# Kernel optimization log

Hardware: AMD Instinct MI355X
Metric: run time of the kernel (lower is better)

Reference implementation:

```python
import jax, jax.numpy as jnp
import numpy as np

NUM_WIRES = 20
DEPTH = 4


def setup_inputs() -> dict:
    key = jax.random.key(0)
    x = jax.random.normal(key, (NUM_WIRES,), dtype=jnp.float32)
    return {"x": x}


def _apply_1q(state, gate, wire):
    # state: flat [2^n] complex; apply 2x2 gate on `wire`
    s = state.reshape(2 ** wire, 2, -1)
    return jnp.einsum('ab,ibj->iaj', gate, s).reshape(-1)


def _apply_cnot(state, control):
    # CNOT on adjacent wires (control, control+1): flip target where control==1
    s = state.reshape(2 ** control, 2, 2, -1)
    s = jnp.concatenate([s[:, :1], s[:, 1:, ::-1]], axis=1)
    return s.reshape(-1)


def _simulate(x):
    n = NUM_WIRES
    state = jnp.zeros(2 ** n, dtype=jnp.complex64).at[0].set(1.0)
    half = (x.astype(jnp.float32) * 0.5)
    c = jnp.cos(half).astype(jnp.complex64)  # [n]
    s = jnp.sin(half).astype(jnp.complex64)  # [n]
    for _ in range(DEPTH):
        for w in range(n):
            cw, sw = c[w], s[w]
            rx = jnp.stack([jnp.stack([cw, -1j * sw]), jnp.stack([-1j * sw, cw])])
            ry = jnp.stack([jnp.stack([cw, -sw]), jnp.stack([sw, cw])])
            state = _apply_1q(state, rx, w)
            state = _apply_1q(state, ry, w)
        for w in range(n - 1):
            state = _apply_cnot(state, w)
    probs = jnp.abs(state) ** 2  # real float32 [2^n]
    expz = []
    for i in range(n):
        p = probs.reshape(2 ** i, 2, -1).sum(axis=(0, 2))
        expz.append(p[0] - p[1])
    return jnp.stack(expz).astype(jnp.float32)  # [n] <Z_i>


def reference(x):
    return _simulate(x)
```

## Files before the change

### kernel.cpp

```cpp
#include <hip/hip_runtime.h>


#define NW 20

__device__ __forceinline__ float2 cmul(float2 a, float2 b) {
    return make_float2(a.x*b.x - a.y*b.y, a.x*b.y + a.y*b.x);
}

__device__ __forceinline__ void apply_gate(float2& a0, float2& a1,
                                           float2 u00, float2 u01,
                                           float2 u10, float2 u11) {
    float2 b0, b1;
    b0.x = u00.x*a0.x - u00.y*a0.y + u01.x*a1.x - u01.y*a1.y;
    b0.y = u00.x*a0.y + u00.y*a0.x + u01.x*a1.y + u01.y*a1.x;
    b1.x = u10.x*a0.x - u10.y*a0.y + u11.x*a1.x - u11.y*a1.y;
    b1.y = u10.x*a0.y + u10.y*a0.x + u11.x*a1.y + u11.y*a1.x;
    a0 = b0; a1 = b1;
}

__device__ __forceinline__ float2 shflx(float2 v, int m) {
    float2 r;
    r.x = __shfl_xor(v.x, m, 64);
    r.y = __shfl_xor(v.y, m, 64);
    return r;
}

__device__ __forceinline__ unsigned sfx(unsigned x) {
    x ^= x >> 1; x ^= x >> 2; x ^= x >> 4; x ^= x >> 8; x ^= x >> 16; return x;
}

template<int A>
__device__ __forceinline__ void gate_regbit(float2 (&amp)[4], const float2* Gw) {
    float2 u00 = Gw[0], u01 = Gw[1], u10 = Gw[2], u11 = Gw[3];
    #pragma unroll
    for (int r = 0; r < 4; r++)
        if (!(r & (1 << A)))
            apply_gate(amp[r], amp[r | (1 << A)], u00, u01, u10, u11);
}

template<int A, int LM>
__device__ __forceinline__ void swap_reg_lane4(float2 (&amp)[4], unsigned lane) {
    bool hb = (lane & (unsigned)LM) != 0u;
    #pragma unroll
    for (int r = 0; r < 4; r++) {
        if (!(r & (1 << A))) {
            float2 lo = amp[r], hi = amp[r | (1 << A)];
            float2 xs = hb ? lo : hi;
            float2 ys = shflx(xs, LM);
            amp[r]            = hb ? ys : lo;
            amp[r | (1 << A)] = hb ? hi : ys;
        }
    }
}

__device__ __forceinline__ void prep_Gs(const float* __restrict__ x, float2* Gs,
                                        unsigned t) {
    if (t < NW) {
        float h = 0.5f * x[t];
        float c = cosf(h), s = sinf(h);
        float cc = c*c, ss = s*s, cs = c*s;
        Gs[t*4+0] = make_float2(cc,  ss);
        Gs[t*4+1] = make_float2(-cs, -cs);
        Gs[t*4+2] = make_float2(cs,  -cs);
        Gs[t*4+3] = make_float2(cc,  -ss);
    }
}

template<int MODE>
__global__ __launch_bounds__(1024) void stageA(const float* __restrict__ x,
                                               const float2* __restrict__ src,
                                               float2* __restrict__ dst) {
    __shared__ float2 lds[4096];
    __shared__ float2 Gs[4*NW];
    const unsigned t = threadIdx.x;
    const unsigned lane = t & 63u, wv = t >> 6;
    const unsigned w0 = wv & 1u, w1 = (wv >> 1) & 1u, w2 = (wv >> 2) & 1u, w3 = wv >> 3;
    const unsigned l4v = (lane >> 4) & 1u, l5v = lane >> 5;
    const unsigned H   = blockIdx.x;
    const unsigned Hp  = H ^ (H >> 1);
    const unsigned inj = (H & 1u) << 11;
    const unsigned lb  = (wv << 8) | (lane << 2);
    const unsigned gb  = (lb ^ (lb >> 1)) ^ inj;

    float4 q0, q1;
    if (MODE == 1) {
        const float4* q = (const float4*)(src + ((size_t)Hp << 12) + (gb & ~3u));
        q0 = q[0]; q1 = q[1];
    }
    prep_Gs(x, Gs, t);
    __syncthreads();

    float2 amp[4];
    if (MODE == 1) {
        float2 e0 = make_float2(q0.x,q0.y), e1 = make_float2(q0.z,q0.w);
        float2 e2 = make_float2(q1.x,q1.y), e3 = make_float2(q1.z,q1.w);
        bool s2 = (gb & 2u) != 0u;
        amp[0] = s2 ? e2 : e0;
        amp[1] = s2 ? e3 : e1;
        amp[2] = s2 ? e1 : e3;
        amp[3] = s2 ? e0 : e2;
    } else {
        float2 P = make_float2(1.0f, 0.0f);
        #pragma unroll
        for (int b = 12; b <= 19; b++)
            P = cmul(P, Gs[(19-b)*4 + (int)((Hp >> (b-12)) & 1u)*2]);
        #pragma unroll
        for (int b = 2; b <= 11; b++)
            P = cmul(P, Gs[(19-b)*4 + (int)((gb >> b) & 1u)*2]);
        float2 T[4];
        #pragma unroll
        for (int j = 0; j < 4; j++)
            T[j] = cmul(P, cmul(Gs[19*4 + (j&1)*2], Gs[18*4 + ((j>>1)&1)*2]));
        bool s2 = (gb & 2u) != 0u;
        amp[0] = s2 ? T[2] : T[0];
        amp[1] = s2 ? T[3] : T[1];
        amp[2] = s2 ? T[1] : T[3];
        amp[3] = s2 ? T[0] : T[2];
    }

    gate_regbit<0>(amp, Gs + 19*4);
    gate_regbit<1>(amp, Gs + 18*4);
    swap_reg_lane4<0,1>(amp, lane);
    swap_reg_lane4<1,2>(amp, lane);
    gate_regbit<0>(amp, Gs + 17*4);
    gate_regbit<1>(amp, Gs + 16*4);
    swap_reg_lane4<0,4>(amp, lane);
    swap_reg_lane4<1,8>(amp, lane);
    gate_regbit<0>(amp, Gs + 15*4);
    gate_regbit<1>(amp, Gs + 14*4);
    swap_reg_lane4<0,16>(amp, lane);
    swap_reg_lane4<1,32>(amp, lane);
    gate_regbit<0>(amp, Gs + 13*4);
    gate_regbit<1>(amp, Gs + 12*4);
    #pragma unroll
    for (int k = 0; k < 4; k++) lds[lane | ((unsigned)k << 6) | (wv << 8)] = amp[k];
    __syncthreads();
    #pragma unroll
    for (int k = 0; k < 4; k++)
        amp[k] = lds[(lane & 15u) | (w0 << 4) | (w1 << 5) | (w2 << 6) | (w3 << 7)
                     | ((unsigned)(k & 1) << 8) | ((unsigned)(k >> 1) << 9)
                     | (l4v << 10) | (l5v << 11)];
    gate_regbit<0>(amp, Gs + 11*4);
    gate_regbit<1>(amp, Gs + 10*4);
    swap_reg_lane4<0,16>(amp, lane);
    gate_regbit<0>(amp, Gs + 9*4);
    swap_reg_lane4<1,32>(amp, lane);
    gate_regbit<1>(amp, Gs + 8*4);
    float2* d = dst + ((size_t)H << 12);
    #pragma unroll
    for (int k = 0; k < 4; k++)
        d[(lane & 15u) | (w0 << 4) | (w1 << 5) | (w2 << 6) | (w3 << 7)
          | (l4v << 8) | (l5v << 9)
          | ((unsigned)(k & 1) << 10) | ((unsigned)(k >> 1) << 11)] = amp[k];
}

template<int FUSE>
__global__ __launch_bounds__(1024) void stageB(const float* __restrict__ x,
                                               float2* __restrict__ st,
                                               float* __restrict__ partial) {
    __shared__ float2 lds[4096];
    __shared__ float2 Gs[4*NW];
    const unsigned t = threadIdx.x;
    const unsigned lane = t & 63u, wv = t >> 6;
    const unsigned w0 = wv & 1u, w1 = (wv >> 1) & 1u, w2 = (wv >> 2) & 1u, w3 = wv >> 3;
    const unsigned m = lane & 15u, l4v = (lane >> 4) & 1u, l5v = lane >> 5;
    const unsigned bb = blockIdx.x;

    float2 amp[4];
    const unsigned lbase = m | (bb << 4) | (l4v << 14) | (l5v << 15)
                         | (w0 << 16) | (w1 << 17) | (w2 << 18) | (w3 << 19);
    #pragma unroll
    for (int k = 0; k < 4; k++)
        amp[k] = st[lbase | ((unsigned)(k & 1) << 12) | ((unsigned)(k >> 1) << 13)];
    prep_Gs(x, Gs, t);
    __syncthreads();

    gate_regbit<0>(amp, Gs + 7*4);
    gate_regbit<1>(amp, Gs + 6*4);
    swap_reg_lane4<0,16>(amp, lane);
    swap_reg_lane4<1,32>(amp, lane);
    gate_regbit<0>(amp, Gs + 5*4);
    gate_regbit<1>(amp, Gs + 4*4);
    #pragma unroll
    for (int k = 0; k < 4; k++) lds[lane | ((unsigned)k << 6) | (wv << 8)] = amp[k];
    __syncthreads();
    #pragma unroll
    for (int k = 0; k < 4; k++)
        amp[k] = lds[(lane & 15u) | (w0 << 4) | (w1 << 5) | (w2 << 6) | (w3 << 7)
                     | ((unsigned)(k & 1) << 8) | ((unsigned)(k >> 1) << 9)
                     | (l4v << 10) | (l5v << 11)];
    gate_regbit<0>(amp, Gs + 3*4);
    gate_regbit<1>(amp, Gs + 2*4);
    swap_reg_lane4<0,16>(amp, lane);
    gate_regbit<0>(amp, Gs + 1*4);
    swap_reg_lane4<1,32>(amp, lane);
    gate_regbit<1>(amp, Gs + 0*4);

    if (!FUSE) {
        #pragma unroll
        for (int k = 0; k < 4; k++)
            st[m | (bb << 4) | (w0 << 12) | (w1 << 13) | (w2 << 14) | (w3 << 15)
               | (l4v << 16) | (l5v << 17)
               | ((unsigned)(k & 1) << 18) | ((unsigned)(k >> 1) << 19)] = amp[k];
    } else {
        float p[4];
        #pragma unroll
        for (int k = 0; k < 4; k++) p[k] = amp[k].x*amp[k].x + amp[k].y*amp[k].y;
        float S19 = (p[0] + p[1]) - (p[2] + p[3]);
        float D   = p[0] - p[1] - p[2] + p[3];
        unsigned v = m | (bb << 4) | (w0 << 12) | (w1 << 13) | (w2 << 14)
                   | (w3 << 15) | (l4v << 16) | (l5v << 17);
        unsigned cm = sfx(v);
        float acc[NW];
        acc[0] = S19; acc[1] = D;
        #pragma unroll
        for (int w = 2; w < NW; w++)
            acc[w] = ((cm >> (19 - w)) & 1u) ? -D : D;

        __syncthreads();
        float* red = (float*)lds;
        #pragma unroll
        for (int w = 0; w < NW; w++) {
            float s = acc[w];
            #pragma unroll
            for (int off = 32; off; off >>= 1) s += __shfl_down(s, off, 64);
            if (lane == 0) red[wv*NW + w] = s;
        }
        __syncthreads();
        if (t < NW) {
            float s = 0.0f;
            #pragma unroll
            for (int v16 = 0; v16 < 16; v16++) s += red[v16*NW + (int)t];
            partial[bb*NW + t] = s;
        }
    }
}

__global__ __launch_bounds__(256) void reduce_out(const float* __restrict__ partial,
                                                  float* __restrict__ out) {
    __shared__ float red[4*NW];
    unsigned t = threadIdx.x;
    float vals[NW];
    #pragma unroll
    for (int w = 0; w < NW; w++) vals[w] = partial[t*NW + w];
    #pragma unroll
    for (int w = 0; w < NW; w++) {
        float v = vals[w];
        #pragma unroll
        for (int off = 32; off; off >>= 1) v += __shfl_down(v, off, 64);
        if ((t & 63u) == 0u) red[(t >> 6)*NW + w] = v;
    }
    __syncthreads();
    if (t < NW) out[t] = red[t] + red[NW+t] + red[2*NW+t] + red[3*NW+t];
}

extern "C" void kernel_launch(void* const* d_in, const int* in_sizes, int n_in,
                              void* d_out, int out_size, void* d_ws, size_t ws_size,
                              hipStream_t stream) {
    (void)in_sizes; (void)n_in; (void)out_size; (void)ws_size;
    const float* x = (const float*)d_in[0];
    float* out = (float*)d_out;

    char* ws = (char*)d_ws;
    float*  partial = (float*)(ws + 1024);
    float2* buf0    = (float2*)(ws + 65536);
    float2* buf1    = (float2*)(ws + 65536 + (size_t)(8u << 20));

    stageA<0><<<256, 1024, 0, stream>>>(x, buf1 , buf0);
    stageB<0><<<256, 1024, 0, stream>>>(x, buf0, nullptr);
    stageA<1><<<256, 1024, 0, stream>>>(x, buf0, buf1);
    stageB<0><<<256, 1024, 0, stream>>>(x, buf1, nullptr);
    stageA<1><<<256, 1024, 0, stream>>>(x, buf1, buf0);
    stageB<1><<<256, 1024, 0, stream>>>(x, buf0, partial);
    reduce_out<<<1, 256, 0, stream>>>(partial, out);
}
```

Baseline: 73.37 us.

## Remap qubit-to-lane layout for vectorized global access and swizzled LDS transposes

Reworks the bit-to-thread mapping in both stages. Stage B now loads and stores state with float4 accesses on paired amplitudes and applies gates only on register bit 1, with more lane swaps. Its LDS transpose gets an XOR swizzle to avoid bank conflicts. Stage A replaces lane shuffles with a second LDS transpose so its global writes are contiguous per lane. The aim is to cut global memory transactions and LDS bank conflicts, at the cost of an extra barrier and LDS round trip in stage A and changed reduction bookkeeping in the fused path.

```diff
diff --git a/kernel.cpp b/kernel.cpp
--- a/kernel.cpp
+++ b/kernel.cpp
@@ -66,6 +66,10 @@
     }
 }
 
+__device__ __forceinline__ unsigned swz(unsigned a) {
+    return a ^ (((a >> 9) & 7u) << 3);
+}
+
 template<int MODE>
 __global__ __launch_bounds__(1024) void stageA(const float* __restrict__ x,
                                                const float2* __restrict__ src,
@@ -75,7 +79,6 @@
     const unsigned t = threadIdx.x;
     const unsigned lane = t & 63u, wv = t >> 6;
     const unsigned w0 = wv & 1u, w1 = (wv >> 1) & 1u, w2 = (wv >> 2) & 1u, w3 = wv >> 3;
-    const unsigned l4v = (lane >> 4) & 1u, l5v = lane >> 5;
     const unsigned H   = blockIdx.x;
     const unsigned Hp  = H ^ (H >> 1);
     const unsigned inj = (H & 1u) << 11;
@@ -137,21 +140,22 @@
     __syncthreads();
     #pragma unroll
     for (int k = 0; k < 4; k++)
-        amp[k] = lds[(lane & 15u) | (w0 << 4) | (w1 << 5) | (w2 << 6) | (w3 << 7)
-                     | ((unsigned)(k & 1) << 8) | ((unsigned)(k >> 1) << 9)
-                     | (l4v << 10) | (l5v << 11)];
+        amp[k] = lds[lane | (w0 << 6) | (w1 << 7) | ((unsigned)k << 8) | (w2 << 10) | (w3 << 11)];
     gate_regbit<0>(amp, Gs + 11*4);
     gate_regbit<1>(amp, Gs + 10*4);
-    swap_reg_lane4<0,16>(amp, lane);
+    __syncthreads();
+    #pragma unroll
+    for (int k = 0; k < 4; k++) lds[lane | ((unsigned)k << 6) | (wv << 8)] = amp[k];
+    __syncthreads();
+    #pragma unroll
+    for (int k = 0; k < 4; k++)
+        amp[k] = lds[lane | (w2 << 6) | (w3 << 7) | (w0 << 8) | (w1 << 9) | ((unsigned)k << 10)];
     gate_regbit<0>(amp, Gs + 9*4);
-    swap_reg_lane4<1,32>(amp, lane);
     gate_regbit<1>(amp, Gs + 8*4);
     float2* d = dst + ((size_t)H << 12);
     #pragma unroll
     for (int k = 0; k < 4; k++)
-        d[(lane & 15u) | (w0 << 4) | (w1 << 5) | (w2 << 6) | (w3 << 7)
-          | (l4v << 8) | (l5v << 9)
-          | ((unsigned)(k & 1) << 10) | ((unsigned)(k >> 1) << 11)] = amp[k];
+        d[lane | (w0 << 6) | (w1 << 7) | (w2 << 8) | (w3 << 9) | ((unsigned)k << 10)] = amp[k];
 }
 
 template<int FUSE>
@@ -163,59 +167,68 @@
     const unsigned t = threadIdx.x;
     const unsigned lane = t & 63u, wv = t >> 6;
     const unsigned w0 = wv & 1u, w1 = (wv >> 1) & 1u, w2 = (wv >> 2) & 1u, w3 = wv >> 3;
-    const unsigned m = lane & 15u, l4v = (lane >> 4) & 1u, l5v = lane >> 5;
+    const unsigned l012 = lane & 7u;
+    const unsigned l3 = (lane >> 3) & 1u, l4 = (lane >> 4) & 1u, l5 = lane >> 5;
     const unsigned bb = blockIdx.x;
 
+    float4 qa, qb;
+    {
+        const unsigned ba = (l012 << 1) | (bb << 4) | (l3 << 13) | (l4 << 14)
+                          | (l5 << 15) | (w0 << 16) | (w1 << 17) | (w2 << 18) | (w3 << 19);
+        qa = *(const float4*)(st + ba);
+        qb = *(const float4*)(st + (ba | (1u << 12)));
+    }
+    prep_Gs(x, Gs, t);
+    __syncthreads();
+
     float2 amp[4];
-    const unsigned lbase = m | (bb << 4) | (l4v << 14) | (l5v << 15)
-                         | (w0 << 16) | (w1 << 17) | (w2 << 18) | (w3 << 19);
-    #pragma unroll
-    for (int k = 0; k < 4; k++)
-        amp[k] = st[lbase | ((unsigned)(k & 1) << 12) | ((unsigned)(k >> 1) << 13)];
-    prep_Gs(x, Gs, t);
-    __syncthreads();
-
-    gate_regbit<0>(amp, Gs + 7*4);
+    amp[0] = make_float2(qa.x, qa.y); amp[1] = make_float2(qa.z, qa.w);
+    amp[2] = make_float2(qb.x, qb.y); amp[3] = make_float2(qb.z, qb.w);
+
+    gate_regbit<1>(amp, Gs + 7*4);
+    swap_reg_lane4<1,8>(amp, lane);
     gate_regbit<1>(amp, Gs + 6*4);
-    swap_reg_lane4<0,16>(amp, lane);
+    swap_reg_lane4<1,16>(amp, lane);
+    gate_regbit<1>(amp, Gs + 5*4);
     swap_reg_lane4<1,32>(amp, lane);
-    gate_regbit<0>(amp, Gs + 5*4);
     gate_regbit<1>(amp, Gs + 4*4);
     #pragma unroll
-    for (int k = 0; k < 4; k++) lds[lane | ((unsigned)k << 6) | (wv << 8)] = amp[k];
-    __syncthreads();
-    #pragma unroll
-    for (int k = 0; k < 4; k++)
-        amp[k] = lds[(lane & 15u) | (w0 << 4) | (w1 << 5) | (w2 << 6) | (w3 << 7)
-                     | ((unsigned)(k & 1) << 8) | ((unsigned)(k >> 1) << 9)
-                     | (l4v << 10) | (l5v << 11)];
-    gate_regbit<0>(amp, Gs + 3*4);
+    for (int k = 0; k < 4; k++)
+        lds[swz(lane | ((unsigned)k << 6) | (wv << 8))] = amp[k];
+    __syncthreads();
+    #pragma unroll
+    for (int k = 0; k < 4; k++)
+        amp[k] = lds[swz(l012 | (w0 << 3) | (w1 << 4) | (w2 << 5)
+                         | ((unsigned)(k & 1) << 6) | (w3 << 7)
+                         | ((unsigned)(k >> 1) << 8)
+                         | (l3 << 9) | (l4 << 10) | (l5 << 11))];
+    gate_regbit<1>(amp, Gs + 3*4);
+    swap_reg_lane4<1,8>(amp, lane);
     gate_regbit<1>(amp, Gs + 2*4);
-    swap_reg_lane4<0,16>(amp, lane);
-    gate_regbit<0>(amp, Gs + 1*4);
+    swap_reg_lane4<1,16>(amp, lane);
+    gate_regbit<1>(amp, Gs + 1*4);
     swap_reg_lane4<1,32>(amp, lane);
     gate_regbit<1>(amp, Gs + 0*4);
 
+    const unsigned sb = (l012 << 1) | (bb << 4) | (w0 << 12) | (w1 << 13)
+                      | (w2 << 14) | (w3 << 15) | (l3 << 16) | (l4 << 17) | (l5 << 18);
     if (!FUSE) {
-        #pragma unroll
-        for (int k = 0; k < 4; k++)
-            st[m | (bb << 4) | (w0 << 12) | (w1 << 13) | (w2 << 14) | (w3 << 15)
-               | (l4v << 16) | (l5v << 17)
-               | ((unsigned)(k & 1) << 18) | ((unsigned)(k >> 1) << 19)] = amp[k];
+        *(float4*)(st + sb) =
+            make_float4(amp[0].x, amp[0].y, amp[1].x, amp[1].y);
+        *(float4*)(st + (sb | (1u << 19))) =
+            make_float4(amp[2].x, amp[2].y, amp[3].x, amp[3].y);
     } else {
         float p[4];
         #pragma unroll
         for (int k = 0; k < 4; k++) p[k] = amp[k].x*amp[k].x + amp[k].y*amp[k].y;
-        float S19 = (p[0] + p[1]) - (p[2] + p[3]);
-        float D   = p[0] - p[1] - p[2] + p[3];
-        unsigned v = m | (bb << 4) | (w0 << 12) | (w1 << 13) | (w2 << 14)
-                   | (w3 << 15) | (l4v << 16) | (l5v << 17);
-        unsigned cm = sfx(v);
+        const float E = (p[0] + p[1]) - (p[2] + p[3]);
+        const float D = p[0] - p[1] - p[2] + p[3];
+        const unsigned cm = sfx(sb);
         float acc[NW];
-        acc[0] = S19; acc[1] = D;
-        #pragma unroll
-        for (int w = 2; w < NW; w++)
-            acc[w] = ((cm >> (19 - w)) & 1u) ? -D : D;
+        #pragma unroll
+        for (int w = 0; w < 19; w++)
+            acc[w] = ((cm >> (19 - w)) & 1u) ? -E : E;
+        acc[19] = (cm & 1u) ? -D : D;
 
         __syncthreads();
         float* red = (float*)lds;
```

Measured after the change: 67.87 us. 1.08x faster.
